# Optimization experiments

Measured on AMD Instinct MI355X. Metric: run time of the kernel, lower is better.

Reference implementation:

```python
import jax, jax.numpy as jnp
import numpy as np

B, T, D, HS = 8, 2048, 1024, 64


def setup_inputs() -> dict:
    key = jax.random.key(0)
    ks = jax.random.split(key, 7)
    return {
        "x": jax.random.normal(ks[0], (B, T, D), dtype=jnp.float32),
        "Wq": jax.random.normal(ks[1], (D, HS), dtype=jnp.float32) / np.sqrt(D),
        "bq": jax.random.normal(ks[2], (HS,), dtype=jnp.float32) * 0.01,
        "Wk": jax.random.normal(ks[3], (D, HS), dtype=jnp.float32) / np.sqrt(D),
        "bk": jax.random.normal(ks[4], (HS,), dtype=jnp.float32) * 0.01,
        "Wv": jax.random.normal(ks[5], (D, HS), dtype=jnp.float32) / np.sqrt(D),
        "bv": jax.random.normal(ks[6], (HS,), dtype=jnp.float32) * 0.01,
    }


def reference(x, Wq, bq, Wk, bk, Wv, bv):
    # Q,K,V projections: [B,T,D] @ [D,HS] -> [B,T,HS]
    Q = x @ Wq + bq
    K = x @ Wk + bk
    V = x @ Wv + bv
    # raw scores [B,T,T]
    scores = jnp.einsum("bqh,bkh->bqk", Q, K)
    # causal mask applied BEFORE scaling (as in the original; -inf is scale-invariant)
    causal = jnp.tril(jnp.ones((T, T), dtype=bool))
    scores = jnp.where(causal[None, :, :], scores, -jnp.inf)
    scores = scores / jnp.sqrt(jnp.asarray(HS, dtype=scores.dtype))
    attn = jax.nn.softmax(scores, axis=-1)
    # dropout is identity in eval mode (deterministic reference)
    return jnp.einsum("bqk,bkh->bqh", attn, V)
```

## Files before the change

### kernel.cpp

```cpp
#include <hip/hip_runtime.h>
#include <hip/hip_bf16.h>

typedef __bf16 bf16x8 __attribute__((ext_vector_type(8)));
typedef __bf16 bf16x4 __attribute__((ext_vector_type(4)));
typedef float  f32x4  __attribute__((ext_vector_type(4)));

#define B_  8
#define T_  2048
#define D_  1024
#define HS_ 64


__global__ __launch_bounds__(256) void pack_w(
    const float* __restrict__ Wq, const float* __restrict__ Wk,
    const float* __restrict__ Wv, __bf16* __restrict__ Wp)
{
    const int t    = blockIdx.x * 256 + threadIdx.x;
    const int lane = t & 63;
    const int pg   = t >> 6;
    const int s    = pg & 3;
    const int c    = (pg >> 2) & 31;
    const int p    = pg >> 7;
    const int m16  = lane & 15;
    const int quad = lane >> 4;

    const float* W = (p == 0) ? Wq : (p == 1) ? Wk : Wv;
    const float* src = W + (size_t)(c * 32 + quad * 8) * 64 + s * 16 + m16;
    bf16x8 frag;
    #pragma unroll
    for (int j = 0; j < 8; ++j) frag[j] = (__bf16)src[(size_t)j * 64];
    *(bf16x8*)(Wp + (size_t)pg * 512 + lane * 8) = frag;
}

__global__ __launch_bounds__(256) void qkv_fused(
    const float* __restrict__ x,
    const __bf16* __restrict__ Wp,
    const float* __restrict__ bq, const float* __restrict__ bk,
    const float* __restrict__ bv,
    __bf16* __restrict__ Q,
    __bf16* __restrict__ Kp,
    __bf16* __restrict__ Vp)
{
    __shared__ alignas(16) unsigned char Smem[73728];

    const int rt   = blockIdx.x;
    const int wave = threadIdx.x >> 6;
    const int lane = threadIdx.x & 63;
    const int m16  = lane & 15;
    const int quad = lane >> 4;
    const int row0 = rt * 32;

    __bf16* Xs = (__bf16*)(Smem + wave * 16896);

    {
        const float* xsrc = x + (size_t)row0 * 1024 + wave * 256;
        const int sr = lane >> 5;
        const int sc = (lane & 31) * 8;
        #pragma unroll
        for (int i = 0; i < 16; ++i) {
            const int r = i * 2 + sr;
            f32x4 v0 = *(const f32x4*)(xsrc + (size_t)r * 1024 + sc);
            f32x4 v1 = *(const f32x4*)(xsrc + (size_t)r * 1024 + sc + 4);
            bf16x8 w;
            #pragma unroll
            for (int e = 0; e < 4; ++e) { w[e] = (__bf16)v0[e]; w[4 + e] = (__bf16)v1[e]; }
            *(bf16x8*)&Xs[r * 264 + sc] = w;
        }
    }
    __builtin_amdgcn_wave_barrier();

    f32x4 acc[3][4][2];
    #pragma unroll
    for (int p = 0; p < 3; ++p)
        #pragma unroll
        for (int s = 0; s < 4; ++s)
            #pragma unroll
            for (int t = 0; t < 2; ++t) acc[p][s][t] = {0.f, 0.f, 0.f, 0.f};

    for (int k0 = 0; k0 < 256; k0 += 32) {
        bf16x8 a0 = *(const bf16x8*)&Xs[m16 * 264 + k0 + quad * 8];
        bf16x8 a1 = *(const bf16x8*)&Xs[(16 + m16) * 264 + k0 + quad * 8];
        const int cbase = wave * 8 + (k0 >> 5);

        bf16x8 bf[12];
        #pragma unroll
        for (int ps = 0; ps < 12; ++ps) {
            const int p = ps >> 2, s = ps & 3;
            bf[ps] = *(const bf16x8*)(Wp +
                ((size_t)((p * 32 + cbase) * 4 + s) << 9) + lane * 8);
        }
        __builtin_amdgcn_sched_barrier(0);

        #pragma unroll
        for (int ps = 0; ps < 12; ++ps) {
            acc[ps >> 2][ps & 3][0] =
                __builtin_amdgcn_mfma_f32_16x16x32_bf16(a0, bf[ps], acc[ps >> 2][ps & 3][0], 0, 0, 0);
            acc[ps >> 2][ps & 3][1] =
                __builtin_amdgcn_mfma_f32_16x16x32_bf16(a1, bf[ps], acc[ps >> 2][ps & 3][1], 0, 0, 0);
        }
    }

    f32x4* Red = (f32x4*)Smem;
    __syncthreads();
    if (wave != 0) {
        #pragma unroll
        for (int p = 0; p < 3; ++p)
            #pragma unroll
            for (int s = 0; s < 4; ++s)
                #pragma unroll
                for (int t = 0; t < 2; ++t)
                    Red[((wave - 1) * 24 + (p * 4 + s) * 2 + t) * 64 + lane] = acc[p][s][t];
    }
    __syncthreads();
    if (wave != 0) return;

    #pragma unroll
    for (int p = 0; p < 3; ++p)
        #pragma unroll
        for (int s = 0; s < 4; ++s)
            #pragma unroll
            for (int t = 0; t < 2; ++t) {
                f32x4 sum = acc[p][s][t];
                #pragma unroll
                for (int w = 0; w < 3; ++w) {
                    f32x4 v = Red[(w * 24 + (p * 4 + s) * 2 + t) * 64 + lane];
                    #pragma unroll
                    for (int e = 0; e < 4; ++e) sum[e] += v[e];
                }
                acc[p][s][t] = sum;
            }

    #pragma unroll
    for (int t = 0; t < 2; ++t) {
        const int row0t = row0 + t * 16;

        #pragma unroll
        for (int s = 0; s < 4; ++s) {
            const int h = s * 16 + m16;
            const float bia = bq[h];
            #pragma unroll
            for (int r = 0; r < 4; ++r)
                Q[(size_t)(row0t + quad * 4 + r) * 64 + h] = (__bf16)(acc[0][s][t][r] + bia);
        }

        const int tb = (row0t >> 4) & 3;
        const int jt = (row0t >> 6) & 31;
        const int bb = row0t >> 11;
        __bf16* kpt = Kp + (((size_t)bb * 32 + jt) * 8) * 512;
        __bf16* vpt = Vp + (((size_t)bb * 32 + jt) * 8) * 512;

        {
            const int snb  = ((tb >> 1) << 1) | (quad & 1);
            const int m16b = ((tb & 1) << 3) | ((quad >> 1) << 2);
            #pragma unroll
            for (int s = 0; s < 4; ++s) {
                const int h = s * 16 + m16;
                const float bia = bk[h];
                const int g     = snb * 2 + (s >> 1);
                const int quadc = ((s & 1) << 1) | (m16 >> 3);
                const int j     = m16 & 7;
                #pragma unroll
                for (int r = 0; r < 4; ++r)
                    kpt[(size_t)g * 512 + (quadc * 16 + m16b + r) * 8 + j] =
                        (__bf16)(acc[1][s][t][r] + bia);
            }
        }
        {
            const int lanec = ((((tb & 1) << 1) | (quad >> 1)) << 4) + m16;
            const int jbase = (quad & 1) << 2;
            #pragma unroll
            for (int s = 0; s < 4; ++s) {
                const int h = s * 16 + m16;
                const float bia = bv[h];
                const int g = s * 2 + (tb >> 1);
                bf16x4 pack;
                #pragma unroll
                for (int r = 0; r < 4; ++r) pack[r] = (__bf16)(acc[2][s][t][r] + bia);
                *(bf16x4*)(vpt + (size_t)g * 512 + lanec * 8 + jbase) = pack;
            }
        }
    }
}

__global__ __launch_bounds__(256) void attn_fused(
    const __bf16* __restrict__ Q,
    const __bf16* __restrict__ Kp,
    const __bf16* __restrict__ Vp,
    float* __restrict__ O)
{
    __shared__ float Mrg[3][64][20];

    const int p  = blockIdx.x;
    const int b  = blockIdx.y;
    const int wave = threadIdx.x >> 6;
    const int lane = threadIdx.x & 63;
    const int m16  = lane & 15;
    const int quad = lane >> 4;
    const float SC = 0.18033688f;

    const __bf16* Qb = Q  + (size_t)b * T_ * HS_;
    const __bf16* Kb = Kp + (size_t)b * 32 * 4096;
    const __bf16* Vb = Vp + (size_t)b * 32 * 4096;
    float* Obase     = O  + (size_t)b * T_ * HS_;

#define LOADT(KA, VA, JT)                                                  \
    {                                                                      \
        const __bf16* kb_ = Kb + (size_t)(JT) * 4096 + lane * 8;           \
        const __bf16* vb_ = Vb + (size_t)(JT) * 4096 + lane * 8;           \
        _Pragma("unroll")                                                  \
        for (int g_ = 0; g_ < 8; ++g_) {                                   \
            KA[g_] = *(const bf16x8*)(kb_ + g_ * 512);                     \
            VA[g_] = *(const bf16x8*)(vb_ + g_ * 512);                     \
        }                                                                  \
    }

#define STEP(CK, CV, NK, NV)                                               \
    {                                                                      \
        const int j0 = jt * 64;                                            \
        f32x4 sv[4];                                                       \
        _Pragma("unroll")                                                  \
        for (int sn_ = 0; sn_ < 4; ++sn_) {                                \
            sv[sn_] = {0.f, 0.f, 0.f, 0.f};                                \
            sv[sn_] = __builtin_amdgcn_mfma_f32_16x16x32_bf16(CK[sn_*2],   qb0, sv[sn_], 0, 0, 0); \
            sv[sn_] = __builtin_amdgcn_mfma_f32_16x16x32_bf16(CK[sn_*2+1], qb1, sv[sn_], 0, 0, 0); \
        }                                                                  \
        if (jt + 4 < ntiles) LOADT(NK, NV, jt + 4);                        \
        __builtin_amdgcn_sched_barrier(0);                                 \
        if (jt == ntiles - 1) {            \
            _Pragma("unroll")                                              \
            for (int sn_ = 0; sn_ < 4; ++sn_) {                            \
                const int kbase = j0 + ((sn_ >> 1) << 5) + (quad << 3) + ((sn_ & 1) << 2); \
                _Pragma("unroll")                                          \
                for (int r_ = 0; r_ < 4; ++r_)                             \
                    sv[sn_][r_] = (kbase + r_ <= qrow) ? sv[sn_][r_] : -3e38f; \
            }                                                              \
        }                                                                  \
        float mx = -3e38f;                                                 \
        _Pragma("unroll")                                                  \
        for (int sn_ = 0; sn_ < 4; ++sn_)                                  \
            _Pragma("unroll")                                              \
            for (int r_ = 0; r_ < 4; ++r_) mx = fmaxf(mx, sv[sn_][r_]);    \
        mx = fmaxf(mx, __shfl_xor(mx, 16));                                \
        mx = fmaxf(mx, __shfl_xor(mx, 32));                                \
        const float newm  = fmaxf(m_run, mx);                              \
        const float alpha = exp2f((m_run - newm) * SC);                    \
        m_run = newm;                                                      \
        const float nm = newm * SC;                                        \
        float rs = 0.f;                                                    \
        _Pragma("unroll")                                                  \
        for (int sn_ = 0; sn_ < 4; ++sn_)                                  \
            _Pragma("unroll")                                              \
            for (int r_ = 0; r_ < 4; ++r_) {                               \
                float pv_ = exp2f(__builtin_fmaf(sv[sn_][r_], SC, -nm));   \
                sv[sn_][r_] = pv_;                                         \
                rs += pv_;                                                 \
            }                                                              \
        rs += __shfl_xor(rs, 16);                                          \
        rs += __shfl_xor(rs, 32);                                          \
        l_run = l_run * alpha + rs;                                        \
        _Pragma("unroll")                                                  \
        for (int hs_ = 0; hs_ < 4; ++hs_)                                  \
            _Pragma("unroll")                                              \
            for (int r_ = 0; r_ < 4; ++r_) o[hs_][r_] *= alpha;            \
        bf16x8 pb0, pb1;                                                   \
        _Pragma("unroll")                                                  \
        for (int r_ = 0; r_ < 4; ++r_) {                                   \
            pb0[r_]     = (__bf16)sv[0][r_];                               \
            pb0[4 + r_] = (__bf16)sv[1][r_];                               \
            pb1[r_]     = (__bf16)sv[2][r_];                               \
            pb1[4 + r_] = (__bf16)sv[3][r_];                               \
        }                                                                  \
        _Pragma("unroll")                                                  \
        for (int hs_ = 0; hs_ < 4; ++hs_) {                                \
            o[hs_] = __builtin_amdgcn_mfma_f32_16x16x32_bf16(CV[hs_*2],   pb0, o[hs_], 0, 0, 0); \
            o[hs_] = __builtin_amdgcn_mfma_f32_16x16x32_bf16(CV[hs_*2+1], pb1, o[hs_], 0, 0, 0); \
        }                                                                  \
    }

    auto runPhase = [&](const int h) {
        const int ntiles = (h >> 2) + 1;
        const int qrow   = h * 16 + m16;

        bf16x8 qb0 = *(const bf16x8*)(Qb + (size_t)qrow * 64 + quad * 8);
        bf16x8 qb1 = *(const bf16x8*)(Qb + (size_t)qrow * 64 + 32 + quad * 8);

        f32x4 o[4];
        #pragma unroll
        for (int hs = 0; hs < 4; ++hs) o[hs] = {0.f, 0.f, 0.f, 0.f};
        float m_run = -3e38f, l_run = 0.f;

        bf16x8 kA[8], vA[8], kB[8], vB[8];
        int jt = wave;
        if (jt < ntiles) {
            LOADT(kA, vA, jt);
            while (true) {
                STEP(kA, vA, kB, vB);
                jt += 4; if (jt >= ntiles) break;
                STEP(kB, vB, kA, vA);
                jt += 4; if (jt >= ntiles) break;
            }
        }

        if (wave != 0) {
            #pragma unroll
            for (int hs = 0; hs < 4; ++hs)
                #pragma unroll
                for (int r = 0; r < 4; ++r) Mrg[wave - 1][lane][hs * 4 + r] = o[hs][r];
            Mrg[wave - 1][lane][16] = m_run;
            Mrg[wave - 1][lane][17] = l_run;
        }
        __syncthreads();
        if (wave == 0) {
            float mw[3], lw[3];
            #pragma unroll
            for (int w = 0; w < 3; ++w) {
                mw[w] = Mrg[w][lane][16];
                lw[w] = Mrg[w][lane][17];
            }
            float M = fmaxf(fmaxf(m_run, mw[0]), fmaxf(mw[1], mw[2]));
            const float a0 = exp2f((m_run - M) * SC);
            float aw[3];
            float den = l_run * a0;
            #pragma unroll
            for (int w = 0; w < 3; ++w) {
                aw[w] = exp2f((mw[w] - M) * SC);
                den += lw[w] * aw[w];
            }
            const float inv = 1.f / den;
            float* Ob = Obase + (size_t)qrow * 64;
            #pragma unroll
            for (int hs = 0; hs < 4; ++hs) {
                f32x4 v;
                #pragma unroll
                for (int r = 0; r < 4; ++r) {
                    float acc = o[hs][r] * a0;
                    #pragma unroll
                    for (int w = 0; w < 3; ++w)
                        acc += Mrg[w][lane][hs * 4 + r] * aw[w];
                    v[r] = acc * inv;
                }
                *(f32x4*)(Ob + hs * 16 + quad * 4) = v;
            }
        }
        __syncthreads();
    };

    runPhase(p);
    runPhase(127 - p);
#undef STEP
#undef LOADT
}

extern "C" void kernel_launch(void* const* d_in, const int* in_sizes, int n_in,
                              void* d_out, int out_size, void* d_ws, size_t ws_size,
                              hipStream_t stream)
{
    const float* x  = (const float*)d_in[0];
    const float* Wq = (const float*)d_in[1];
    const float* bq = (const float*)d_in[2];
    const float* Wk = (const float*)d_in[3];
    const float* bk = (const float*)d_in[4];
    const float* Wv = (const float*)d_in[5];
    const float* bv = (const float*)d_in[6];
    float* out = (float*)d_out;

    __bf16* Wp = (__bf16*)d_ws;
    __bf16* Q  = Wp + 384 * 512;
    __bf16* Kp = Q  + (size_t)B_ * T_ * HS_;
    __bf16* Vp = Kp + (size_t)B_ * T_ * HS_;

    pack_w<<<96, 256, 0, stream>>>(Wq, Wk, Wv, Wp);
    qkv_fused<<<512, 256, 0, stream>>>(x, Wp, bq, bk, bv, Q, Kp, Vp);
    attn_fused<<<dim3(64, 8), 256, 0, stream>>>(Q, Kp, Vp, out);
}
```

Baseline: 130.9 us.

## Double-buffer QKV weight loads; process 32 query rows over 8 waves in attention

In the QKV projection kernel, weight fragments are now double-buffered so the next k-step's global loads are issued before the current MFMAs run, hiding load latency. The attention kernel changes from 4 waves handling 16 query rows to 8 waves (512 threads) handling two 16-row groups. Each loaded K/V tile is therefore reused for twice as many queries, and the key tiles are split across more waves. V loads are also no longer prefetched a stage ahead, and the grid halves to 256 blocks. The trade-offs are higher register pressure, fewer blocks across the CUs, and an 8-way merge through a larger shared buffer.

```diff
diff --git a/kernel.cpp b/kernel.cpp
--- a/kernel.cpp
+++ b/kernel.cpp
@@ -77,28 +77,42 @@
             #pragma unroll
             for (int t = 0; t < 2; ++t) acc[p][s][t] = {0.f, 0.f, 0.f, 0.f};
 
-    for (int k0 = 0; k0 < 256; k0 += 32) {
-        bf16x8 a0 = *(const bf16x8*)&Xs[m16 * 264 + k0 + quad * 8];
-        bf16x8 a1 = *(const bf16x8*)&Xs[(16 + m16) * 264 + k0 + quad * 8];
-        const int cbase = wave * 8 + (k0 >> 5);
-
-        bf16x8 bf[12];
-        #pragma unroll
-        for (int ps = 0; ps < 12; ++ps) {
-            const int p = ps >> 2, s = ps & 3;
-            bf[ps] = *(const bf16x8*)(Wp +
-                ((size_t)((p * 32 + cbase) * 4 + s) << 9) + lane * 8);
-        }
-        __builtin_amdgcn_sched_barrier(0);
-
-        #pragma unroll
-        for (int ps = 0; ps < 12; ++ps) {
-            acc[ps >> 2][ps & 3][0] =
-                __builtin_amdgcn_mfma_f32_16x16x32_bf16(a0, bf[ps], acc[ps >> 2][ps & 3][0], 0, 0, 0);
-            acc[ps >> 2][ps & 3][1] =
-                __builtin_amdgcn_mfma_f32_16x16x32_bf16(a1, bf[ps], acc[ps >> 2][ps & 3][1], 0, 0, 0);
-        }
-    }
+    bf16x8 bfA[12], bfB[12];
+
+#define WLOAD(BUF, K0)                                                     \
+    {                                                                      \
+        const int cb_ = wave * 8 + ((K0) >> 5);                            \
+        _Pragma("unroll")                                                  \
+        for (int ps_ = 0; ps_ < 12; ++ps_) {                               \
+            const int p_ = ps_ >> 2, s_ = ps_ & 3;                         \
+            BUF[ps_] = *(const bf16x8*)(Wp +                               \
+                ((size_t)((p_ * 32 + cb_) * 4 + s_) << 9) + lane * 8);     \
+        }                                                                  \
+    }
+#define KSTEP(BUF, K0)                                                     \
+    {                                                                      \
+        bf16x8 a0 = *(const bf16x8*)&Xs[m16 * 264 + (K0) + quad * 8];      \
+        bf16x8 a1 = *(const bf16x8*)&Xs[(16 + m16) * 264 + (K0) + quad * 8]; \
+        __builtin_amdgcn_sched_barrier(0);                                 \
+        _Pragma("unroll")                                                  \
+        for (int ps_ = 0; ps_ < 12; ++ps_) {                               \
+            acc[ps_ >> 2][ps_ & 3][0] =                                    \
+                __builtin_amdgcn_mfma_f32_16x16x32_bf16(a0, BUF[ps_], acc[ps_ >> 2][ps_ & 3][0], 0, 0, 0); \
+            acc[ps_ >> 2][ps_ & 3][1] =                                    \
+                __builtin_amdgcn_mfma_f32_16x16x32_bf16(a1, BUF[ps_], acc[ps_ >> 2][ps_ & 3][1], 0, 0, 0); \
+        }                                                                  \
+    }
+
+    WLOAD(bfA, 0);
+    #pragma unroll
+    for (int k0 = 0; k0 < 256; k0 += 64) {
+        WLOAD(bfB, k0 + 32);
+        KSTEP(bfA, k0);
+        if (k0 + 64 < 256) WLOAD(bfA, k0 + 64);
+        KSTEP(bfB, k0 + 32);
+    }
+#undef KSTEP
+#undef WLOAD
 
     f32x4* Red = (f32x4*)Smem;
     __syncthreads();
@@ -182,15 +196,15 @@
     }
 }
 
-__global__ __launch_bounds__(256) void attn_fused(
+__global__ __launch_bounds__(512) void attn_fused(
     const __bf16* __restrict__ Q,
     const __bf16* __restrict__ Kp,
     const __bf16* __restrict__ Vp,
     float* __restrict__ O)
 {
-    __shared__ float Mrg[3][64][20];
-
-    const int p  = blockIdx.x;
+    __shared__ float Mrg[8][64][37];
+
+    const int s  = blockIdx.x;
     const int b  = blockIdx.y;
     const int wave = threadIdx.x >> 6;
     const int lane = threadIdx.x & 63;
@@ -203,126 +217,162 @@
     const __bf16* Vb = Vp + (size_t)b * 32 * 4096;
     float* Obase     = O  + (size_t)b * T_ * HS_;
 
-#define LOADT(KA, VA, JT)                                                  \
+    bf16x8 vA[8];
+
+#define LOADK(KA, JT)                                                      \
     {                                                                      \
         const __bf16* kb_ = Kb + (size_t)(JT) * 4096 + lane * 8;           \
+        _Pragma("unroll")                                                  \
+        for (int g_ = 0; g_ < 8; ++g_) KA[g_] = *(const bf16x8*)(kb_ + g_ * 512); \
+    }
+#define LOADV(JT)                                                          \
+    {                                                                      \
         const __bf16* vb_ = Vb + (size_t)(JT) * 4096 + lane * 8;           \
         _Pragma("unroll")                                                  \
-        for (int g_ = 0; g_ < 8; ++g_) {                                   \
-            KA[g_] = *(const bf16x8*)(kb_ + g_ * 512);                     \
-            VA[g_] = *(const bf16x8*)(vb_ + g_ * 512);                     \
-        }                                                                  \
-    }
-
-#define STEP(CK, CV, NK, NV)                                               \
+        for (int g_ = 0; g_ < 8; ++g_) vA[g_] = *(const bf16x8*)(vb_ + g_ * 512); \
+    }
+
+#define STEP(CK, NK)                                                       \
     {                                                                      \
         const int j0 = jt * 64;                                            \
-        f32x4 sv[4];                                                       \
+        LOADV(jt);                       \
+        f32x4 svA[4], svB[4];                                              \
         _Pragma("unroll")                                                  \
         for (int sn_ = 0; sn_ < 4; ++sn_) {                                \
-            sv[sn_] = {0.f, 0.f, 0.f, 0.f};                                \
-            sv[sn_] = __builtin_amdgcn_mfma_f32_16x16x32_bf16(CK[sn_*2],   qb0, sv[sn_], 0, 0, 0); \
-            sv[sn_] = __builtin_amdgcn_mfma_f32_16x16x32_bf16(CK[sn_*2+1], qb1, sv[sn_], 0, 0, 0); \
-        }                                                                  \
-        if (jt + 4 < ntiles) LOADT(NK, NV, jt + 4);                        \
+            svA[sn_] = {0.f, 0.f, 0.f, 0.f};                               \
+            svB[sn_] = {0.f, 0.f, 0.f, 0.f};                               \
+            svA[sn_] = __builtin_amdgcn_mfma_f32_16x16x32_bf16(CK[sn_*2],   qA0, svA[sn_], 0, 0, 0); \
+            svA[sn_] = __builtin_amdgcn_mfma_f32_16x16x32_bf16(CK[sn_*2+1], qA1, svA[sn_], 0, 0, 0); \
+            svB[sn_] = __builtin_amdgcn_mfma_f32_16x16x32_bf16(CK[sn_*2],   qB0, svB[sn_], 0, 0, 0); \
+            svB[sn_] = __builtin_amdgcn_mfma_f32_16x16x32_bf16(CK[sn_*2+1], qB1, svB[sn_], 0, 0, 0); \
+        }                                                                  \
+        if (jt + 8 < ntiles) LOADK(NK, jt + 8);                            \
         __builtin_amdgcn_sched_barrier(0);                                 \
-        if (jt == ntiles - 1) {            \
+        if (jt == ntiles - 1) {    \
             _Pragma("unroll")                                              \
             for (int sn_ = 0; sn_ < 4; ++sn_) {                            \
                 const int kbase = j0 + ((sn_ >> 1) << 5) + (quad << 3) + ((sn_ & 1) << 2); \
                 _Pragma("unroll")                                          \
-                for (int r_ = 0; r_ < 4; ++r_)                             \
-                    sv[sn_][r_] = (kbase + r_ <= qrow) ? sv[sn_][r_] : -3e38f; \
+                for (int r_ = 0; r_ < 4; ++r_) {                           \
+                    svA[sn_][r_] = (kbase + r_ <= qrowA) ? svA[sn_][r_] : -3e38f; \
+                    svB[sn_][r_] = (kbase + r_ <= qrowB) ? svB[sn_][r_] : -3e38f; \
+                }                                                          \
             }                                                              \
         }                                                                  \
-        float mx = -3e38f;                                                 \
-        _Pragma("unroll")                                                  \
-        for (int sn_ = 0; sn_ < 4; ++sn_)                                  \
-            _Pragma("unroll")                                              \
-            for (int r_ = 0; r_ < 4; ++r_) mx = fmaxf(mx, sv[sn_][r_]);    \
-        mx = fmaxf(mx, __shfl_xor(mx, 16));                                \
-        mx = fmaxf(mx, __shfl_xor(mx, 32));                                \
-        const float newm  = fmaxf(m_run, mx);                              \
-        const float alpha = exp2f((m_run - newm) * SC);                    \
-        m_run = newm;                                                      \
-        const float nm = newm * SC;                                        \
-        float rs = 0.f;                                                    \
+        float mxA = -3e38f, mxB = -3e38f;                                  \
         _Pragma("unroll")                                                  \
         for (int sn_ = 0; sn_ < 4; ++sn_)                                  \
             _Pragma("unroll")                                              \
             for (int r_ = 0; r_ < 4; ++r_) {                               \
-                float pv_ = exp2f(__builtin_fmaf(sv[sn_][r_], SC, -nm));   \
-                sv[sn_][r_] = pv_;                                         \
-                rs += pv_;                                                 \
+                mxA = fmaxf(mxA, svA[sn_][r_]);                            \
+                mxB = fmaxf(mxB, svB[sn_][r_]);                            \
             }                                                              \
-        rs += __shfl_xor(rs, 16);                                          \
-        rs += __shfl_xor(rs, 32);                                          \
-        l_run = l_run * alpha + rs;                                        \
+        mxA = fmaxf(mxA, __shfl_xor(mxA, 16));                             \
+        mxA = fmaxf(mxA, __shfl_xor(mxA, 32));                             \
+        mxB = fmaxf(mxB, __shfl_xor(mxB, 16));                             \
+        mxB = fmaxf(mxB, __shfl_xor(mxB, 32));                             \
+        const float newmA = fmaxf(mA, mxA);                                \
+        const float newmB = fmaxf(mB, mxB);                                \
+        const float alA = exp2f((mA - newmA) * SC);                        \
+        const float alB = exp2f((mB - newmB) * SC);                        \
+        mA = newmA; mB = newmB;                                            \
+        const float nmA = newmA * SC, nmB = newmB * SC;                    \
+        float rsA = 0.f, rsB = 0.f;                                        \
+        _Pragma("unroll")                                                  \
+        for (int sn_ = 0; sn_ < 4; ++sn_)                                  \
+            _Pragma("unroll")                                              \
+            for (int r_ = 0; r_ < 4; ++r_) {                               \
+                float pa_ = exp2f(__builtin_fmaf(svA[sn_][r_], SC, -nmA)); \
+                float pb_ = exp2f(__builtin_fmaf(svB[sn_][r_], SC, -nmB)); \
+                svA[sn_][r_] = pa_; rsA += pa_;                            \
+                svB[sn_][r_] = pb_; rsB += pb_;                            \
+            }                                                              \
+        rsA += __shfl_xor(rsA, 16); rsA += __shfl_xor(rsA, 32);            \
+        rsB += __shfl_xor(rsB, 16); rsB += __shfl_xor(rsB, 32);            \
+        lA = lA * alA + rsA;  lB = lB * alB + rsB;                         \
         _Pragma("unroll")                                                  \
         for (int hs_ = 0; hs_ < 4; ++hs_)                                  \
             _Pragma("unroll")                                              \
-            for (int r_ = 0; r_ < 4; ++r_) o[hs_][r_] *= alpha;            \
-        bf16x8 pb0, pb1;                                                   \
+            for (int r_ = 0; r_ < 4; ++r_) {                               \
+                oA[hs_][r_] *= alA;                                        \
+                oB[hs_][r_] *= alB;                                        \
+            }                                                              \
+        bf16x8 pA0, pA1, pB0, pB1;                                         \
         _Pragma("unroll")                                                  \
         for (int r_ = 0; r_ < 4; ++r_) {                                   \
-            pb0[r_]     = (__bf16)sv[0][r_];                               \
-            pb0[4 + r_] = (__bf16)sv[1][r_];                               \
-            pb1[r_]     = (__bf16)sv[2][r_];                               \
-            pb1[4 + r_] = (__bf16)sv[3][r_];                               \
+            pA0[r_]     = (__bf16)svA[0][r_];                              \
+            pA0[4 + r_] = (__bf16)svA[1][r_];                              \
+            pA1[r_]     = (__bf16)svA[2][r_];                              \
+            pA1[4 + r_] = (__bf16)svA[3][r_];                              \
+            pB0[r_]     = (__bf16)svB[0][r_];                              \
+            pB0[4 + r_] = (__bf16)svB[1][r_];                              \
+            pB1[r_]     = (__bf16)svB[2][r_];                              \
+            pB1[4 + r_] = (__bf16)svB[3][r_];                              \
         }                                                                  \
         _Pragma("unroll")                                                  \
         for (int hs_ = 0; hs_ < 4; ++hs_) {                                \
-            o[hs_] = __builtin_amdgcn_mfma_f32_16x16x32_bf16(CV[hs_*2],   pb0, o[hs_], 0, 0, 0); \
-            o[hs_] = __builtin_amdgcn_mfma_f32_16x16x32_bf16(CV[hs_*2+1], pb1, o[hs_], 0, 0, 0); \
-        }                                                                  \
-    }
-
-    auto runPhase = [&](const int h) {
-        const int ntiles = (h >> 2) + 1;
-        const int qrow   = h * 16 + m16;
-
-        bf16x8 qb0 = *(const bf16x8*)(Qb + (size_t)qrow * 64 + quad * 8);
-        bf16x8 qb1 = *(const bf16x8*)(Qb + (size_t)qrow * 64 + 32 + quad * 8);
-
-        f32x4 o[4];
-        #pragma unroll
-        for (int hs = 0; hs < 4; ++hs) o[hs] = {0.f, 0.f, 0.f, 0.f};
-        float m_run = -3e38f, l_run = 0.f;
-
-        bf16x8 kA[8], vA[8], kB[8], vB[8];
+            oA[hs_] = __builtin_amdgcn_mfma_f32_16x16x32_bf16(vA[hs_*2],   pA0, oA[hs_], 0, 0, 0); \
+            oA[hs_] = __builtin_amdgcn_mfma_f32_16x16x32_bf16(vA[hs_*2+1], pA1, oA[hs_], 0, 0, 0); \
+            oB[hs_] = __builtin_amdgcn_mfma_f32_16x16x32_bf16(vA[hs_*2],   pB0, oB[hs_], 0, 0, 0); \
+            oB[hs_] = __builtin_amdgcn_mfma_f32_16x16x32_bf16(vA[hs_*2+1], pB1, oB[hs_], 0, 0, 0); \
+        }                                                                  \
+    }
+
+    auto runPhase = [&](const int f) {
+        const int ntiles = (f >> 1) + 1;
+        const int qrowA  = f * 32 + m16;
+        const int qrowB  = qrowA + 16;
+
+        bf16x8 qA0 = *(const bf16x8*)(Qb + (size_t)qrowA * 64 + quad * 8);
+        bf16x8 qA1 = *(const bf16x8*)(Qb + (size_t)qrowA * 64 + 32 + quad * 8);
+        bf16x8 qB0 = *(const bf16x8*)(Qb + (size_t)qrowB * 64 + quad * 8);
+        bf16x8 qB1 = *(const bf16x8*)(Qb + (size_t)qrowB * 64 + 32 + quad * 8);
+
+        f32x4 oA[4], oB[4];
+        #pragma unroll
+        for (int hs = 0; hs < 4; ++hs) {
+            oA[hs] = {0.f, 0.f, 0.f, 0.f};
+            oB[hs] = {0.f, 0.f, 0.f, 0.f};
+        }
+        float mA = -3e38f, lA = 0.f, mB = -3e38f, lB = 0.f;
+
+        bf16x8 kA[8], kB[8];
         int jt = wave;
         if (jt < ntiles) {
-            LOADT(kA, vA, jt);
+            LOADK(kA, jt);
             while (true) {
-                STEP(kA, vA, kB, vB);
-                jt += 4; if (jt >= ntiles) break;
-                STEP(kB, vB, kA, vA);
-                jt += 4; if (jt >= ntiles) break;
-            }
-        }
-
-        if (wave != 0) {
-            #pragma unroll
-            for (int hs = 0; hs < 4; ++hs)
-                #pragma unroll
-                for (int r = 0; r < 4; ++r) Mrg[wave - 1][lane][hs * 4 + r] = o[hs][r];
-            Mrg[wave - 1][lane][16] = m_run;
-            Mrg[wave - 1][lane][17] = l_run;
-        }
+                STEP(kA, kB);
+                jt += 8; if (jt >= ntiles) break;
+                STEP(kB, kA);
+                jt += 8; if (jt >= ntiles) break;
+            }
+        }
+
+        #pragma unroll
+        for (int hs = 0; hs < 4; ++hs)
+            #pragma unroll
+            for (int r = 0; r < 4; ++r) {
+                Mrg[wave][lane][hs * 4 + r]      = oA[hs][r];
+                Mrg[wave][lane][18 + hs * 4 + r] = oB[hs][r];
+            }
+        Mrg[wave][lane][16] = mA; Mrg[wave][lane][17] = lA;
+        Mrg[wave][lane][34] = mB; Mrg[wave][lane][35] = lB;
         __syncthreads();
-        if (wave == 0) {
-            float mw[3], lw[3];
-            #pragma unroll
-            for (int w = 0; w < 3; ++w) {
-                mw[w] = Mrg[w][lane][16];
-                lw[w] = Mrg[w][lane][17];
-            }
-            float M = fmaxf(fmaxf(m_run, mw[0]), fmaxf(mw[1], mw[2]));
-            const float a0 = exp2f((m_run - M) * SC);
-            float aw[3];
-            float den = l_run * a0;
-            #pragma unroll
-            for (int w = 0; w < 3; ++w) {
+        if (wave < 2) {
+            const int off  = wave * 18;
+            const int qrow = f * 32 + wave * 16 + m16;
+            float mw[8], lw[8];
+            #pragma unroll
+            for (int w = 0; w < 8; ++w) {
+                mw[w] = Mrg[w][lane][off + 16];
+                lw[w] = Mrg[w][lane][off + 17];
+            }
+            float M = mw[0];
+            #pragma unroll
+            for (int w = 1; w < 8; ++w) M = fmaxf(M, mw[w]);
+            float aw[8], den = 0.f;
+            #pragma unroll
+            for (int w = 0; w < 8; ++w) {
                 aw[w] = exp2f((mw[w] - M) * SC);
                 den += lw[w] * aw[w];
             }
@@ -333,10 +383,10 @@
                 f32x4 v;
                 #pragma unroll
                 for (int r = 0; r < 4; ++r) {
-                    float acc = o[hs][r] * a0;
+                    float acc = 0.f;
                     #pragma unroll
-                    for (int w = 0; w < 3; ++w)
-                        acc += Mrg[w][lane][hs * 4 + r] * aw[w];
+                    for (int w = 0; w < 8; ++w)
+                        acc += Mrg[w][lane][off + hs * 4 + r] * aw[w];
                     v[r] = acc * inv;
                 }
                 *(f32x4*)(Ob + hs * 16 + quad * 4) = v;
@@ -345,10 +395,11 @@
         __syncthreads();
     };
 
-    runPhase(p);
-    runPhase(127 - p);
+    runPhase(s);
+    runPhase(63 - s);
 #undef STEP
-#undef LOADT
+#undef LOADV
+#undef LOADK
 }
 
 extern "C" void kernel_launch(void* const* d_in, const int* in_sizes, int n_in,
@@ -371,5 +422,5 @@
 
     pack_w<<<96, 256, 0, stream>>>(Wq, Wk, Wv, Wp);
     qkv_fused<<<512, 256, 0, stream>>>(x, Wp, bq, bk, bv, Q, Kp, Vp);
-    attn_fused<<<dim3(64, 8), 256, 0, stream>>>(Q, Kp, Vp, out);
+    attn_fused<<<dim3(32, 8), 512, 0, stream>>>(Q, Kp, Vp, out);
 }
```

New measurement: 128.1 us. -2.2%, faster.

## Split attention into one block per query tile and double-buffer QKV weight loads

Applied to the files above, without the earlier changes.

The attention kernel now launches one block per 16-row query tile (128x8 grid), longest tiles first, instead of pairing tile p with tile 127-p inside each block. K stays double-buffered but V is loaded per step into a single buffer to cut register use, and launch bounds request 3 blocks per SIMD-group for higher occupancy. The QKV projection GEMM double-buffers its weight fragment loads across k-steps so global loads overlap the MFMAs. The risks are exposed V load latency before the PV MFMAs, and load imbalance now left to the hardware scheduler rather than to explicit pairing.

```diff
diff --git a/kernel.cpp b/kernel.cpp
--- a/kernel.cpp
+++ b/kernel.cpp
@@ -77,28 +77,42 @@
             #pragma unroll
             for (int t = 0; t < 2; ++t) acc[p][s][t] = {0.f, 0.f, 0.f, 0.f};
 
-    for (int k0 = 0; k0 < 256; k0 += 32) {
-        bf16x8 a0 = *(const bf16x8*)&Xs[m16 * 264 + k0 + quad * 8];
-        bf16x8 a1 = *(const bf16x8*)&Xs[(16 + m16) * 264 + k0 + quad * 8];
-        const int cbase = wave * 8 + (k0 >> 5);
-
-        bf16x8 bf[12];
-        #pragma unroll
-        for (int ps = 0; ps < 12; ++ps) {
-            const int p = ps >> 2, s = ps & 3;
-            bf[ps] = *(const bf16x8*)(Wp +
-                ((size_t)((p * 32 + cbase) * 4 + s) << 9) + lane * 8);
-        }
-        __builtin_amdgcn_sched_barrier(0);
-
-        #pragma unroll
-        for (int ps = 0; ps < 12; ++ps) {
-            acc[ps >> 2][ps & 3][0] =
-                __builtin_amdgcn_mfma_f32_16x16x32_bf16(a0, bf[ps], acc[ps >> 2][ps & 3][0], 0, 0, 0);
-            acc[ps >> 2][ps & 3][1] =
-                __builtin_amdgcn_mfma_f32_16x16x32_bf16(a1, bf[ps], acc[ps >> 2][ps & 3][1], 0, 0, 0);
-        }
-    }
+    bf16x8 bfA[12], bfB[12];
+
+#define WLOAD(BUF, K0)                                                     \
+    {                                                                      \
+        const int cb_ = wave * 8 + ((K0) >> 5);                            \
+        _Pragma("unroll")                                                  \
+        for (int ps_ = 0; ps_ < 12; ++ps_) {                               \
+            const int p_ = ps_ >> 2, s_ = ps_ & 3;                         \
+            BUF[ps_] = *(const bf16x8*)(Wp +                               \
+                ((size_t)((p_ * 32 + cb_) * 4 + s_) << 9) + lane * 8);     \
+        }                                                                  \
+    }
+#define KSTEP(BUF, K0)                                                     \
+    {                                                                      \
+        bf16x8 a0 = *(const bf16x8*)&Xs[m16 * 264 + (K0) + quad * 8];      \
+        bf16x8 a1 = *(const bf16x8*)&Xs[(16 + m16) * 264 + (K0) + quad * 8]; \
+        __builtin_amdgcn_sched_barrier(0);                                 \
+        _Pragma("unroll")                                                  \
+        for (int ps_ = 0; ps_ < 12; ++ps_) {                               \
+            acc[ps_ >> 2][ps_ & 3][0] =                                    \
+                __builtin_amdgcn_mfma_f32_16x16x32_bf16(a0, BUF[ps_], acc[ps_ >> 2][ps_ & 3][0], 0, 0, 0); \
+            acc[ps_ >> 2][ps_ & 3][1] =                                    \
+                __builtin_amdgcn_mfma_f32_16x16x32_bf16(a1, BUF[ps_], acc[ps_ >> 2][ps_ & 3][1], 0, 0, 0); \
+        }                                                                  \
+    }
+
+    WLOAD(bfA, 0);
+    #pragma unroll
+    for (int k0 = 0; k0 < 256; k0 += 64) {
+        WLOAD(bfB, k0 + 32);
+        KSTEP(bfA, k0);
+        if (k0 + 64 < 256) WLOAD(bfA, k0 + 64);
+        KSTEP(bfB, k0 + 32);
+    }
+#undef KSTEP
+#undef WLOAD
 
     f32x4* Red = (f32x4*)Smem;
     __syncthreads();
@@ -182,7 +196,7 @@
     }
 }
 
-__global__ __launch_bounds__(256) void attn_fused(
+__global__ __launch_bounds__(256, 3) void attn_fused(
     const __bf16* __restrict__ Q,
     const __bf16* __restrict__ Kp,
     const __bf16* __restrict__ Vp,
@@ -190,7 +204,7 @@
 {
     __shared__ float Mrg[3][64][20];
 
-    const int p  = blockIdx.x;
+    const int h  = 127 - blockIdx.x;
     const int b  = blockIdx.y;
     const int wave = threadIdx.x >> 6;
     const int lane = threadIdx.x & 63;
@@ -203,20 +217,36 @@
     const __bf16* Vb = Vp + (size_t)b * 32 * 4096;
     float* Obase     = O  + (size_t)b * T_ * HS_;
 
-#define LOADT(KA, VA, JT)                                                  \
+    const int ntiles = (h >> 2) + 1;
+    const int qrow   = h * 16 + m16;
+
+    bf16x8 qb0 = *(const bf16x8*)(Qb + (size_t)qrow * 64 + quad * 8);
+    bf16x8 qb1 = *(const bf16x8*)(Qb + (size_t)qrow * 64 + 32 + quad * 8);
+
+    f32x4 o[4];
+    #pragma unroll
+    for (int hs = 0; hs < 4; ++hs) o[hs] = {0.f, 0.f, 0.f, 0.f};
+    float m_run = -3e38f, l_run = 0.f;
+
+    bf16x8 kA[8], kB[8], vA[8];
+
+#define LOADK(KA, JT)                                                      \
     {                                                                      \
         const __bf16* kb_ = Kb + (size_t)(JT) * 4096 + lane * 8;           \
+        _Pragma("unroll")                                                  \
+        for (int g_ = 0; g_ < 8; ++g_) KA[g_] = *(const bf16x8*)(kb_ + g_ * 512); \
+    }
+#define LOADV(JT)                                                          \
+    {                                                                      \
         const __bf16* vb_ = Vb + (size_t)(JT) * 4096 + lane * 8;           \
         _Pragma("unroll")                                                  \
-        for (int g_ = 0; g_ < 8; ++g_) {                                   \
-            KA[g_] = *(const bf16x8*)(kb_ + g_ * 512);                     \
-            VA[g_] = *(const bf16x8*)(vb_ + g_ * 512);                     \
-        }                                                                  \
-    }
-
-#define STEP(CK, CV, NK, NV)                                               \
+        for (int g_ = 0; g_ < 8; ++g_) vA[g_] = *(const bf16x8*)(vb_ + g_ * 512); \
+    }
+
+#define STEP(CK, NK)                                                       \
     {                                                                      \
         const int j0 = jt * 64;                                            \
+        LOADV(jt);                       \
         f32x4 sv[4];                                                       \
         _Pragma("unroll")                                                  \
         for (int sn_ = 0; sn_ < 4; ++sn_) {                                \
@@ -224,7 +254,7 @@
             sv[sn_] = __builtin_amdgcn_mfma_f32_16x16x32_bf16(CK[sn_*2],   qb0, sv[sn_], 0, 0, 0); \
             sv[sn_] = __builtin_amdgcn_mfma_f32_16x16x32_bf16(CK[sn_*2+1], qb1, sv[sn_], 0, 0, 0); \
         }                                                                  \
-        if (jt + 4 < ntiles) LOADT(NK, NV, jt + 4);                        \
+        if (jt + 4 < ntiles) LOADK(NK, jt + 4);                            \
         __builtin_amdgcn_sched_barrier(0);                                 \
         if (jt == ntiles - 1) {            \
             _Pragma("unroll")                                              \
@@ -272,83 +302,66 @@
         }                                                                  \
         _Pragma("unroll")                                                  \
         for (int hs_ = 0; hs_ < 4; ++hs_) {                                \
-            o[hs_] = __builtin_amdgcn_mfma_f32_16x16x32_bf16(CV[hs_*2],   pb0, o[hs_], 0, 0, 0); \
-            o[hs_] = __builtin_amdgcn_mfma_f32_16x16x32_bf16(CV[hs_*2+1], pb1, o[hs_], 0, 0, 0); \
-        }                                                                  \
-    }
-
-    auto runPhase = [&](const int h) {
-        const int ntiles = (h >> 2) + 1;
-        const int qrow   = h * 16 + m16;
-
-        bf16x8 qb0 = *(const bf16x8*)(Qb + (size_t)qrow * 64 + quad * 8);
-        bf16x8 qb1 = *(const bf16x8*)(Qb + (size_t)qrow * 64 + 32 + quad * 8);
-
-        f32x4 o[4];
-        #pragma unroll
-        for (int hs = 0; hs < 4; ++hs) o[hs] = {0.f, 0.f, 0.f, 0.f};
-        float m_run = -3e38f, l_run = 0.f;
-
-        bf16x8 kA[8], vA[8], kB[8], vB[8];
-        int jt = wave;
-        if (jt < ntiles) {
-            LOADT(kA, vA, jt);
-            while (true) {
-                STEP(kA, vA, kB, vB);
-                jt += 4; if (jt >= ntiles) break;
-                STEP(kB, vB, kA, vA);
-                jt += 4; if (jt >= ntiles) break;
+            o[hs_] = __builtin_amdgcn_mfma_f32_16x16x32_bf16(vA[hs_*2],   pb0, o[hs_], 0, 0, 0); \
+            o[hs_] = __builtin_amdgcn_mfma_f32_16x16x32_bf16(vA[hs_*2+1], pb1, o[hs_], 0, 0, 0); \
+        }                                                                  \
+    }
+
+    int jt = wave;
+    if (jt < ntiles) {
+        LOADK(kA, jt);
+        while (true) {
+            STEP(kA, kB);
+            jt += 4; if (jt >= ntiles) break;
+            STEP(kB, kA);
+            jt += 4; if (jt >= ntiles) break;
+        }
+    }
+#undef STEP
+#undef LOADV
+#undef LOADK
+
+    if (wave != 0) {
+        #pragma unroll
+        for (int hs = 0; hs < 4; ++hs)
+            #pragma unroll
+            for (int r = 0; r < 4; ++r) Mrg[wave - 1][lane][hs * 4 + r] = o[hs][r];
+        Mrg[wave - 1][lane][16] = m_run;
+        Mrg[wave - 1][lane][17] = l_run;
+    }
+    __syncthreads();
+    if (wave == 0) {
+        float mw[3], lw[3];
+        #pragma unroll
+        for (int w = 0; w < 3; ++w) {
+            mw[w] = Mrg[w][lane][16];
+            lw[w] = Mrg[w][lane][17];
+        }
+        float M = fmaxf(fmaxf(m_run, mw[0]), fmaxf(mw[1], mw[2]));
+        const float a0 = exp2f((m_run - M) * SC);
+        float aw[3];
+        float den = l_run * a0;
+        #pragma unroll
+        for (int w = 0; w < 3; ++w) {
+            aw[w] = exp2f((mw[w] - M) * SC);
+            den += lw[w] * aw[w];
+        }
+        const float inv = 1.f / den;
+        float* Ob = Obase + (size_t)qrow * 64;
+        #pragma unroll
+        for (int hs = 0; hs < 4; ++hs) {
+            f32x4 v;
+            #pragma unroll
+            for (int r = 0; r < 4; ++r) {
+                float acc = o[hs][r] * a0;
+                #pragma unroll
+                for (int w = 0; w < 3; ++w)
+                    acc += Mrg[w][lane][hs * 4 + r] * aw[w];
+                v[r] = acc * inv;
             }
-        }
-
-        if (wave != 0) {
-            #pragma unroll
-            for (int hs = 0; hs < 4; ++hs)
-                #pragma unroll
-                for (int r = 0; r < 4; ++r) Mrg[wave - 1][lane][hs * 4 + r] = o[hs][r];
-            Mrg[wave - 1][lane][16] = m_run;
-            Mrg[wave - 1][lane][17] = l_run;
-        }
-        __syncthreads();
-        if (wave == 0) {
-            float mw[3], lw[3];
-            #pragma unroll
-            for (int w = 0; w < 3; ++w) {
-                mw[w] = Mrg[w][lane][16];
-                lw[w] = Mrg[w][lane][17];
-            }
-            float M = fmaxf(fmaxf(m_run, mw[0]), fmaxf(mw[1], mw[2]));
-            const float a0 = exp2f((m_run - M) * SC);
-            float aw[3];
-            float den = l_run * a0;
-            #pragma unroll
-            for (int w = 0; w < 3; ++w) {
-                aw[w] = exp2f((mw[w] - M) * SC);
-                den += lw[w] * aw[w];
-            }
-            const float inv = 1.f / den;
-            float* Ob = Obase + (size_t)qrow * 64;
-            #pragma unroll
-            for (int hs = 0; hs < 4; ++hs) {
-                f32x4 v;
-                #pragma unroll
-                for (int r = 0; r < 4; ++r) {
-                    float acc = o[hs][r] * a0;
-                    #pragma unroll
-                    for (int w = 0; w < 3; ++w)
-                        acc += Mrg[w][lane][hs * 4 + r] * aw[w];
-                    v[r] = acc * inv;
-                }
-                *(f32x4*)(Ob + hs * 16 + quad * 4) = v;
-            }
-        }
-        __syncthreads();
-    };
-
-    runPhase(p);
-    runPhase(127 - p);
-#undef STEP
-#undef LOADT
+            *(f32x4*)(Ob + hs * 16 + quad * 4) = v;
+        }
+    }
 }
 
 extern "C" void kernel_launch(void* const* d_in, const int* in_sizes, int n_in,
@@ -371,5 +384,5 @@
 
     pack_w<<<96, 256, 0, stream>>>(Wq, Wk, Wv, Wp);
     qkv_fused<<<512, 256, 0, stream>>>(x, Wp, bq, bk, bv, Q, Kp, Vp);
-    attn_fused<<<dim3(64, 8), 256, 0, stream>>>(Q, Kp, Vp, out);
+    attn_fused<<<dim3(128, 8), 256, 0, stream>>>(Q, Kp, Vp, out);
 }
```

Measured after the change: 132.7 us. Within noise of the previous version (+1.4%).
